# Optimization experiments

Measured on AMD Instinct MI355X. Metric: run time of the kernel, lower is better.

The kernel has to match this reference:

```python
import jax, jax.numpy as jnp
import numpy as np

N_NODES = 110
C = 4096  # in_channels = hidden = out_channels


def setup_inputs() -> dict:
    key = jax.random.key(0)
    ks = jax.random.split(key, 8)
    x = jax.random.normal(ks[0], (N_NODES, C), dtype=jnp.float32)
    adj = jax.random.randint(ks[1], (N_NODES, N_NODES), 0, 2, dtype=jnp.int32)
    # torch.nn.Linear weights stored [out_features, in_features]
    W2 = jax.random.normal(ks[2], (C, C), dtype=jnp.float32) / np.sqrt(C)
    b2 = jax.random.normal(ks[3], (C,), dtype=jnp.float32) * 0.01
    W1 = jax.random.normal(ks[4], (2 * C, C), dtype=jnp.float32) / np.sqrt(2 * C)
    b1 = jax.random.normal(ks[5], (C,), dtype=jnp.float32) * 0.01
    Wl = jax.random.normal(ks[6], (N_NODES, N_NODES), dtype=jnp.float32) / np.sqrt(N_NODES)
    bl = jax.random.normal(ks[7], (N_NODES,), dtype=jnp.float32) * 0.01
    # note: W1 is stored [in=2C, out=C]; W2 [in=C, out=C]; Wl [in=110, out=110]
    return {"x": x, "adj": adj, "W2": W2, "b2": b2, "W1": W1, "b1": b1, "Wl": Wl, "bl": bl}


def reference(x, adj, W2, b2, W1, b1, Wl, bl):
    # FeatGraphConv: h = lin2(x)
    h = x @ W2 + b2  # [N, C]
    # edge_index.nonzero(): adjacency -> edge list (i=src, j=dst); mean-aggregate
    # h[src] at dst. Dense equivalent: column-normalized mask matmul.
    mask = (adj != 0).astype(x.dtype)  # [N, N]
    deg = mask.sum(axis=0)  # in-degree of each target node j
    aggr = (mask.T @ h) / jnp.maximum(deg, 1.0)[:, None]  # [N, C]; 0 for isolated nodes (PyG mean)
    # update: lin1(cat(h, aggr)) then relu (in RegGNN.forward)
    out = jax.nn.relu(jnp.concatenate([h, aggr], axis=1) @ W1 + b1)  # [N, C]
    # x.t(); lin(110,110); x.t()
    out = (out.T @ Wl.T + bl).T  # [N, C]
    return out
```

## Files before the change

### kernel.cpp

```cpp
#include <hip/hip_runtime.h>
#include <hip/hip_fp16.h>

#define C 4096
#define NN 110
#define MPAD 112
#define NMT 7
#define KBS (NMT * 512)

typedef _Float16 f16x8 __attribute__((ext_vector_type(8)));
typedef float fx4 __attribute__((ext_vector_type(4)));
typedef unsigned long long ull;


__global__ __launch_bounds__(256)
void prep1_kernel(const float* __restrict__ x, _Float16* __restrict__ A1t) {
    int u = blockIdx.x * 256 + threadIdx.x;
    int kb  = u / 448;
    int rem = u - kb * 448;
    int mt  = rem >> 6;
    int L   = rem & 63;
    int n   = mt * 16 + (L & 15);
    int c   = kb * 32 + (L >> 4) * 8;
    f16x8 hv;
    if (n < NN) {
        float4 v0 = *(const float4*)(x + (size_t)n * C + c);
        float4 v1 = *(const float4*)(x + (size_t)n * C + c + 4);
        hv[0]=(_Float16)v0.x; hv[1]=(_Float16)v0.y; hv[2]=(_Float16)v0.z; hv[3]=(_Float16)v0.w;
        hv[4]=(_Float16)v1.x; hv[5]=(_Float16)v1.y; hv[6]=(_Float16)v1.z; hv[7]=(_Float16)v1.w;
    } else {
        for (int e = 0; e < 8; ++e) hv[e] = (_Float16)0.f;
    }
    *(f16x8*)(A1t + (size_t)u * 8) = hv;
}

__global__ __launch_bounds__(128)
void maskprep_kernel(const int* __restrict__ adj, ull* __restrict__ mlo,
                     ull* __restrict__ mhi, float* __restrict__ degs) {
    int j = threadIdx.x;
    if (j < NN) {
        ull lo = 0, hi = 0; int dg = 0;
        for (int i = 0; i < 64; ++i) {
            int m = (adj[i * NN + j] != 0);
            lo |= ((ull)m) << i; dg += m;
        }
        for (int i = 64; i < NN; ++i) {
            int m = (adj[i * NN + j] != 0);
            hi |= ((ull)m) << (i - 64); dg += m;
        }
        mlo[j] = lo; mhi[j] = hi;
        degs[j] = (float)(dg > 0 ? dg : 1);
    }
}

#define PIPE_BARRIER()                                                \
    do {                                                              \
        asm volatile("s_waitcnt lgkmcnt(0)" ::: "memory");            \
        __builtin_amdgcn_s_barrier();                                 \
        __builtin_amdgcn_sched_barrier(0);                            \
    } while (0)

template<int NITER>
__global__ __launch_bounds__(256, 3)
void mm_kernel(const _Float16* __restrict__ A, const float* __restrict__ B,
               float* __restrict__ Cacc) {
    __shared__ __align__(16) _Float16 As[2][2 * KBS];
    __shared__ __align__(16) _Float16 Bs[2][64 * 64];

    const int t   = threadIdx.x;
    const int j0  = blockIdx.x * 64;
    const int kb0 = blockIdx.y * (NITER * 2);
    const int w   = t >> 6;
    const int L   = t & 63;
    const int l15 = L & 15;
    const int q   = L >> 4;
    const int sc2 = (t & 31) * 2;
    const int kgr = (t >> 5) & 7;

    fx4 acc[7];
#pragma unroll
    for (int mt = 0; mt < 7; ++mt) acc[mt] = (fx4){0.f, 0.f, 0.f, 0.f};

    const float*    Bp  = B + (size_t)blockIdx.y * (NITER * 64) * C + j0 + sc2;
    const _Float16* ApC = A + (size_t)kb0 * KBS;
    const _Float16* BsR = &Bs[0][0] + (w * 16 + l15) * 64;
    const _Float16* AsR = &As[0][0];

    f16x8  av[4];
    float2 bva[8], bvb[8];

#define LOADA(ch)                                                              \
    { _Pragma("unroll")                                                        \
      for (int i = 0; i < 4; ++i)                                              \
          if (i < 3 || t < 128)                                                \
              av[i] = *(const f16x8*)(ApC + (size_t)(ch) * (2 * KBS)           \
                                      + (t + i * 256) * 8); }

#define COMMITA(buf)                                                           \
    { _Pragma("unroll")                                                        \
      for (int i = 0; i < 4; ++i)                                              \
          if (i < 3 || t < 128)                                                \
              *(f16x8*)(&As[buf][0] + (t + i * 256) * 8) = av[i]; }

#define LOADB(dst, ch)                                                         \
    { _Pragma("unroll")                                                        \
      for (int p = 0; p < 8; ++p)                                              \
          dst[p] = *(const float2*)(Bp + (size_t)((ch) * 64 + kgr * 8 + p) * C); }

#define COMMITB(src, buf)                                                      \
    { f16x8 h0, h1;                                                            \
      _Pragma("unroll")                                                        \
      for (int e = 0; e < 8; ++e) { h0[e] = (_Float16)src[e].x;                \
                                    h1[e] = (_Float16)src[e].y; }              \
      *(f16x8*)(&Bs[buf][0] + sc2 * 64 + ((kgr ^ (sc2 & 7)) << 3)) = h0;       \
      *(f16x8*)(&Bs[buf][0] + (sc2 + 1) * 64 + ((kgr ^ ((sc2 + 1) & 7)) << 3)) = h1; }

    LOADA(0);
    LOADB(bva, 0);
    COMMITA(0);
    COMMITB(bva, 0);
    LOADB(bva, 1);
    PIPE_BARRIER();

#pragma unroll
    for (int it = 0; it < NITER; ++it) {
        if (it + 1 < NITER) LOADA(it + 1);
        __builtin_amdgcn_sched_barrier(0);
        if (it + 2 < NITER) {
            if (it & 1) { LOADB(bva, it + 2); } else { LOADB(bvb, it + 2); }
        }
        __builtin_amdgcn_sched_barrier(0);
#pragma unroll
        for (int s = 0; s < 2; ++s) {
            f16x8 bf = *(const f16x8*)(BsR + (it & 1) * 4096
                            + ((((s << 2) + q) ^ (l15 & 7)) << 3));
#pragma unroll
            for (int mt = 0; mt < 7; ++mt) {
                f16x8 afrag = *(const f16x8*)(AsR + (it & 1) * (2 * KBS)
                                  + (s * 7 + mt) * 512 + L * 8);
                acc[mt] = __builtin_amdgcn_mfma_f32_16x16x32_f16(
                    afrag, bf, acc[mt], 0, 0, 0);
            }
        }
        if (it + 1 < NITER) {
            COMMITA((it + 1) & 1);
            if (it & 1) { COMMITB(bvb, (it + 1) & 1); }
            else        { COMMITB(bva, (it + 1) & 1); }
            PIPE_BARRIER();
        }
    }

    const int col = j0 + w * 16 + l15;
#pragma unroll
    for (int mt = 0; mt < 7; ++mt)
#pragma unroll
        for (int r = 0; r < 4; ++r) {
            int row = mt * 16 + q * 4 + r;
            if (row < NN)
                atomicAdd(&Cacc[(size_t)row * C + col], acc[mt][r]);
        }
#undef LOADA
#undef COMMITA
#undef LOADB
#undef COMMITB
}

__device__ __forceinline__ size_t fragidx(int n, int c) {
    return (size_t)(c >> 5) * KBS + (n >> 4) * 512
         + (((c >> 3) & 3) * 16 + (n & 15)) * 8 + (c & 7);
}

__global__ __launch_bounds__(256)
void agg_kernel(const float* __restrict__ h_raw, const ull* __restrict__ gmlo,
                const ull* __restrict__ gmhi, const float* __restrict__ gdegs,
                const float* __restrict__ b2, _Float16* __restrict__ A3t) {
    __shared__ float hb[NN * 16];
    const int t  = threadIdx.x;
    const int c0 = blockIdx.x * 16;

    for (int idx = t; idx < NN * 8; idx += 256) {
        int n = idx >> 3, cp = (idx & 7) << 1;
        float2 v = *(const float2*)(h_raw + (size_t)n * C + c0 + cp);
        float v0 = v.x + b2[c0 + cp];
        float v1 = v.y + b2[c0 + cp + 1];
        hb[n * 16 + cp]     = v0;
        hb[n * 16 + cp + 1] = v1;
        union { _Float16 h[2]; unsigned u; } pk;
        pk.h[0] = (_Float16)v0;
        pk.h[1] = (_Float16)v1;
        *(unsigned*)(A3t + fragidx(n, c0 + cp)) = pk.u;
    }
    if (t < 32) {
        int n  = 110 + ((t >> 3) & 1);
        int hs = t >> 4;
        int cp = (t & 7) << 1;
        *(unsigned*)(A3t + fragidx(n, hs * C + c0 + cp)) = 0u;
    }
    __syncthreads();
    for (int idx = t; idx < NN * 8; idx += 256) {
        int j = idx >> 3, cp = (idx & 7) << 1;
        ull lo = gmlo[j], hi = gmhi[j];
        float dg = gdegs[j];
        float a0 = 0.f, a1 = 0.f;
        for (int i = 0; i < 64; ++i)
            if ((lo >> i) & 1) { a0 += hb[i * 16 + cp]; a1 += hb[i * 16 + cp + 1]; }
        for (int i = 64; i < NN; ++i)
            if ((hi >> (i - 64)) & 1) { a0 += hb[i * 16 + cp]; a1 += hb[i * 16 + cp + 1]; }
        union { _Float16 h[2]; unsigned u; } pk;
        pk.h[0] = (_Float16)(a0 / dg);
        pk.h[1] = (_Float16)(a1 / dg);
        *(unsigned*)(A3t + fragidx(j, C + c0 + cp)) = pk.u;
    }
}

__global__ __launch_bounds__(256)
void fin_kernel(const float* __restrict__ z_raw, const float* __restrict__ b1,
                const float* __restrict__ Wl, const float* __restrict__ bl,
                float* __restrict__ out) {
    __shared__ float zs[NN * 64];
    const int t  = threadIdx.x;
    const int c0 = blockIdx.x * 64;
    const int c  = t & 63;

    for (int idx = t; idx < NN * 64; idx += 256) {
        int k = idx >> 6, cc = idx & 63;
        float v = z_raw[(size_t)k * C + c0 + cc] + b1[c0 + cc];
        zs[idx] = fmaxf(v, 0.f);
    }
    __syncthreads();
    for (int jj = 0; jj < 7; ++jj) {
        int j = blockIdx.y * 28 + jj * 4 + (t >> 6);
        if (j < NN) {
            float a = bl[j];
#pragma unroll 2
            for (int k = 0; k < NN; ++k)
                a += Wl[j * NN + k] * zs[k * 64 + c];
            out[(size_t)j * C + c0 + c] = a;
        }
    }
}

extern "C" void kernel_launch(void* const* d_in, const int* in_sizes, int n_in,
                              void* d_out, int out_size, void* d_ws, size_t ws_size,
                              hipStream_t stream) {
    const float* x   = (const float*)d_in[0];
    const int*   adj = (const int*)d_in[1];
    const float* W2  = (const float*)d_in[2];
    const float* b2  = (const float*)d_in[3];
    const float* W1  = (const float*)d_in[4];
    const float* b1  = (const float*)d_in[5];
    const float* Wl  = (const float*)d_in[6];
    const float* bl  = (const float*)d_in[7];
    float* out = (float*)d_out;

    char* ws = (char*)d_ws;
    float*    h_raw = (float*)(ws);
    float*    z_raw = (float*)(ws + 1802240);
    _Float16* A1t   = (_Float16*)(ws + 3604480);
    _Float16* A3t   = (_Float16*)(ws + 4521984);
    ull*      mlo   = (ull*)(ws + 6356992);
    ull*      mhi   = (ull*)(ws + 6357872);
    float*    degs  = (float*)(ws + 6358752);

    hipMemsetAsync(d_ws, 0, 3604480, stream);
    prep1_kernel<<<224, 256, 0, stream>>>(x, A1t);
    maskprep_kernel<<<1, 128, 0, stream>>>(adj, mlo, mhi, degs);
    mm_kernel<4><<<dim3(64, 16), 256, 0, stream>>>(A1t, W2, h_raw);
    agg_kernel<<<C / 16, 256, 0, stream>>>(h_raw, mlo, mhi, degs, b2, A3t);
    mm_kernel<8><<<dim3(64, 16), 256, 0, stream>>>(A3t, W1, z_raw);
    fin_kernel<<<dim3(C / 64, 4), 256, 0, stream>>>(z_raw, b1, Wl, bl, out);
}
```

Baseline: 355.5 us.

## Replace atomic split-K accumulation with per-slice partial buffers and reduction

The GEMM kernels now write split-K partial results into separate per-slice buffers with plain stores instead of atomicAdd into a zeroed accumulator. The split-K factor drops from 16 to 8, so each block does twice the K iterations. The partials are summed in the aggregation kernel for the first GEMM and in a new reduction kernel for the second. This removes the memset and the atomic contention, but adds an extra kernel launch, more partial-buffer traffic, and halves the grid size (512 blocks), which may leave the device underoccupied.

```diff
diff --git a/kernel.cpp b/kernel.cpp
--- a/kernel.cpp
+++ b/kernel.cpp
@@ -6,6 +6,7 @@
 #define MPAD 112
 #define NMT 7
 #define KBS (NMT * 512)
+#define NSLICE 8
 
 typedef _Float16 f16x8 __attribute__((ext_vector_type(8)));
 typedef float fx4 __attribute__((ext_vector_type(4)));
@@ -62,13 +63,12 @@
 template<int NITER>
 __global__ __launch_bounds__(256, 3)
 void mm_kernel(const _Float16* __restrict__ A, const float* __restrict__ B,
-               float* __restrict__ Cacc) {
+               float* __restrict__ Cpart) {
     __shared__ __align__(16) _Float16 As[2][2 * KBS];
     __shared__ __align__(16) _Float16 Bs[2][64 * 64];
 
     const int t   = threadIdx.x;
     const int j0  = blockIdx.x * 64;
-    const int kb0 = blockIdx.y * (NITER * 2);
     const int w   = t >> 6;
     const int L   = t & 63;
     const int l15 = L & 15;
@@ -81,7 +81,7 @@
     for (int mt = 0; mt < 7; ++mt) acc[mt] = (fx4){0.f, 0.f, 0.f, 0.f};
 
     const float*    Bp  = B + (size_t)blockIdx.y * (NITER * 64) * C + j0 + sc2;
-    const _Float16* ApC = A + (size_t)kb0 * KBS;
+    const _Float16* ApC = A + (size_t)blockIdx.y * (NITER * 2) * KBS;
     const _Float16* BsR = &Bs[0][0] + (w * 16 + l15) * 64;
     const _Float16* AsR = &As[0][0];
 
@@ -149,14 +149,14 @@
         }
     }
 
-    const int col = j0 + w * 16 + l15;
+    float* Cp = Cpart + (size_t)blockIdx.y * (NN * C) + j0 + w * 16 + l15;
 #pragma unroll
     for (int mt = 0; mt < 7; ++mt)
 #pragma unroll
         for (int r = 0; r < 4; ++r) {
             int row = mt * 16 + q * 4 + r;
             if (row < NN)
-                atomicAdd(&Cacc[(size_t)row * C + col], acc[mt][r]);
+                Cp[(size_t)row * C] = acc[mt][r];
         }
 #undef LOADA
 #undef COMMITA
@@ -170,7 +170,7 @@
 }
 
 __global__ __launch_bounds__(256)
-void agg_kernel(const float* __restrict__ h_raw, const ull* __restrict__ gmlo,
+void agg_kernel(const float* __restrict__ hpart, const ull* __restrict__ gmlo,
                 const ull* __restrict__ gmhi, const float* __restrict__ gdegs,
                 const float* __restrict__ b2, _Float16* __restrict__ A3t) {
     __shared__ float hb[NN * 16];
@@ -179,9 +179,13 @@
 
     for (int idx = t; idx < NN * 8; idx += 256) {
         int n = idx >> 3, cp = (idx & 7) << 1;
-        float2 v = *(const float2*)(h_raw + (size_t)n * C + c0 + cp);
-        float v0 = v.x + b2[c0 + cp];
-        float v1 = v.y + b2[c0 + cp + 1];
+        float v0 = b2[c0 + cp], v1 = b2[c0 + cp + 1];
+#pragma unroll
+        for (int p = 0; p < NSLICE; ++p) {
+            float2 v = *(const float2*)(hpart + (size_t)p * (NN * C)
+                                        + (size_t)n * C + c0 + cp);
+            v0 += v.x; v1 += v.y;
+        }
         hb[n * 16 + cp]     = v0;
         hb[n * 16 + cp + 1] = v1;
         union { _Float16 h[2]; unsigned u; } pk;
@@ -213,6 +217,20 @@
 }
 
 __global__ __launch_bounds__(256)
+void zred_kernel(const float* __restrict__ zpart, float* __restrict__ z_raw) {
+    int idx = blockIdx.x * 256 + threadIdx.x;
+    if (idx < NN * (C / 4)) {
+        fx4 s = (fx4){0.f, 0.f, 0.f, 0.f};
+#pragma unroll
+        for (int p = 0; p < NSLICE; ++p) {
+            fx4 v = *(const fx4*)(zpart + (size_t)p * (NN * C) + (size_t)idx * 4);
+            s.x += v.x; s.y += v.y; s.z += v.z; s.w += v.w;
+        }
+        *(fx4*)(z_raw + (size_t)idx * 4) = s;
+    }
+}
+
+__global__ __launch_bounds__(256)
 void fin_kernel(const float* __restrict__ z_raw, const float* __restrict__ b1,
                 const float* __restrict__ Wl, const float* __restrict__ bl,
                 float* __restrict__ out) {
@@ -253,19 +271,20 @@
     float* out = (float*)d_out;
 
     char* ws = (char*)d_ws;
-    float*    h_raw = (float*)(ws);
-    float*    z_raw = (float*)(ws + 1802240);
-    _Float16* A1t   = (_Float16*)(ws + 3604480);
-    _Float16* A3t   = (_Float16*)(ws + 4521984);
-    ull*      mlo   = (ull*)(ws + 6356992);
-    ull*      mhi   = (ull*)(ws + 6357872);
-    float*    degs  = (float*)(ws + 6358752);
-
-    hipMemsetAsync(d_ws, 0, 3604480, stream);
+    float*    hpart = (float*)(ws);
+    float*    zpart = (float*)(ws + 14417920);
+    float*    z_raw = (float*)(ws + 28835840);
+    _Float16* A1t   = (_Float16*)(ws + 30638080);
+    _Float16* A3t   = (_Float16*)(ws + 31555584);
+    ull*      mlo   = (ull*)(ws + 33390592);
+    ull*      mhi   = (ull*)(ws + 33391472);
+    float*    degs  = (float*)(ws + 33392352);
+
     prep1_kernel<<<224, 256, 0, stream>>>(x, A1t);
     maskprep_kernel<<<1, 128, 0, stream>>>(adj, mlo, mhi, degs);
-    mm_kernel<4><<<dim3(64, 16), 256, 0, stream>>>(A1t, W2, h_raw);
-    agg_kernel<<<C / 16, 256, 0, stream>>>(h_raw, mlo, mhi, degs, b2, A3t);
-    mm_kernel<8><<<dim3(64, 16), 256, 0, stream>>>(A3t, W1, z_raw);
+    mm_kernel<8><<<dim3(64, NSLICE), 256, 0, stream>>>(A1t, W2, hpart);
+    agg_kernel<<<C / 16, 256, 0, stream>>>(hpart, mlo, mhi, degs, b2, A3t);
+    mm_kernel<16><<<dim3(64, NSLICE), 256, 0, stream>>>(A3t, W1, zpart);
+    zred_kernel<<<440, 256, 0, stream>>>(zpart, z_raw);
     fin_kernel<<<dim3(C / 64, 4), 256, 0, stream>>>(z_raw, b1, Wl, bl, out);
 }
```

Measured after the change: 352.1 us. Within noise of the previous version (-1.0%).

## Retile GEMM to 256-wide N tiles with register-resident A fragments

Applied to the files above, without the earlier changes.

The mm_kernel is restructured so that each block covers 256 output columns instead of 64, with a K chunk of 32 per iteration. A fragments are loaded straight from global memory into registers rather than staged through LDS, and B is staged as float4 reads converted to fp16 into a swizzled LDS tile. Each wave keeps a 7x4 grid of MFMA accumulators, so each B fragment read from LDS is reused across 7 M-tiles and each A fragment across 4 N-tiles. The mask-prep kernel is folded into an extra block of prep1 to save one launch. The cost is higher register pressure, so occupancy is lowered to 2 blocks per CU, and A is now read redundantly from global memory by every block.

```diff
diff --git a/kernel.cpp b/kernel.cpp
--- a/kernel.cpp
+++ b/kernel.cpp
@@ -3,7 +3,6 @@
 
 #define C 4096
 #define NN 110
-#define MPAD 112
 #define NMT 7
 #define KBS (NMT * 512)
 
@@ -11,9 +10,39 @@
 typedef float fx4 __attribute__((ext_vector_type(4)));
 typedef unsigned long long ull;
 
+__device__ __forceinline__ size_t fragidx(int n, int c) {
+    return (size_t)(c >> 5) * KBS + (n >> 4) * 512
+         + (((c >> 3) & 3) * 16 + (n & 15)) * 8 + (c & 7);
+}
+
+#define PIPE_BARRIER()                                                \
+    do {                                                              \
+        asm volatile("s_waitcnt lgkmcnt(0)" ::: "memory");            \
+        __builtin_amdgcn_s_barrier();                                 \
+        __builtin_amdgcn_sched_barrier(0);                            \
+    } while (0)
 
 __global__ __launch_bounds__(256)
-void prep1_kernel(const float* __restrict__ x, _Float16* __restrict__ A1t) {
+void prep1_kernel(const float* __restrict__ x, _Float16* __restrict__ A1t,
+                  const int* __restrict__ adj, ull* __restrict__ mlo,
+                  ull* __restrict__ mhi, float* __restrict__ degs) {
+    if (blockIdx.x == 224) {
+        int j = threadIdx.x;
+        if (j < NN) {
+            ull lo = 0, hi = 0; int dg = 0;
+            for (int i = 0; i < 64; ++i) {
+                int m = (adj[i * NN + j] != 0);
+                lo |= ((ull)m) << i; dg += m;
+            }
+            for (int i = 64; i < NN; ++i) {
+                int m = (adj[i * NN + j] != 0);
+                hi |= ((ull)m) << (i - 64); dg += m;
+            }
+            mlo[j] = lo; mhi[j] = hi;
+            degs[j] = (float)(dg > 0 ? dg : 1);
+        }
+        return;
+    }
     int u = blockIdx.x * 256 + threadIdx.x;
     int kb  = u / 448;
     int rem = u - kb * 448;
@@ -33,140 +62,95 @@
     *(f16x8*)(A1t + (size_t)u * 8) = hv;
 }
 
-__global__ __launch_bounds__(128)
-void maskprep_kernel(const int* __restrict__ adj, ull* __restrict__ mlo,
-                     ull* __restrict__ mhi, float* __restrict__ degs) {
-    int j = threadIdx.x;
-    if (j < NN) {
-        ull lo = 0, hi = 0; int dg = 0;
-        for (int i = 0; i < 64; ++i) {
-            int m = (adj[i * NN + j] != 0);
-            lo |= ((ull)m) << i; dg += m;
-        }
-        for (int i = 64; i < NN; ++i) {
-            int m = (adj[i * NN + j] != 0);
-            hi |= ((ull)m) << (i - 64); dg += m;
-        }
-        mlo[j] = lo; mhi[j] = hi;
-        degs[j] = (float)(dg > 0 ? dg : 1);
-    }
-}
-
-#define PIPE_BARRIER()                                                \
-    do {                                                              \
-        asm volatile("s_waitcnt lgkmcnt(0)" ::: "memory");            \
-        __builtin_amdgcn_s_barrier();                                 \
-        __builtin_amdgcn_sched_barrier(0);                            \
-    } while (0)
-
-template<int NITER>
-__global__ __launch_bounds__(256, 3)
+template<int NC>
+__global__ __launch_bounds__(256, 2)
 void mm_kernel(const _Float16* __restrict__ A, const float* __restrict__ B,
                float* __restrict__ Cacc) {
-    __shared__ __align__(16) _Float16 As[2][2 * KBS];
-    __shared__ __align__(16) _Float16 Bs[2][64 * 64];
+    __shared__ __align__(16) _Float16 Bs[2][256 * 32];
 
     const int t   = threadIdx.x;
-    const int j0  = blockIdx.x * 64;
-    const int kb0 = blockIdx.y * (NITER * 2);
+    const int n0  = blockIdx.x * 256;
+    const int y   = blockIdx.y;
     const int w   = t >> 6;
     const int L   = t & 63;
     const int l15 = L & 15;
     const int q   = L >> 4;
-    const int sc2 = (t & 31) * 2;
-    const int kgr = (t >> 5) & 7;
-
-    fx4 acc[7];
-#pragma unroll
-    for (int mt = 0; mt < 7; ++mt) acc[mt] = (fx4){0.f, 0.f, 0.f, 0.f};
-
-    const float*    Bp  = B + (size_t)blockIdx.y * (NITER * 64) * C + j0 + sc2;
-    const _Float16* ApC = A + (size_t)kb0 * KBS;
-    const _Float16* BsR = &Bs[0][0] + (w * 16 + l15) * 64;
-    const _Float16* AsR = &As[0][0];
-
-    f16x8  av[4];
-    float2 bva[8], bvb[8];
-
-#define LOADA(ch)                                                              \
-    { _Pragma("unroll")                                                        \
-      for (int i = 0; i < 4; ++i)                                              \
-          if (i < 3 || t < 128)                                                \
-              av[i] = *(const f16x8*)(ApC + (size_t)(ch) * (2 * KBS)           \
-                                      + (t + i * 256) * 8); }
-
-#define COMMITA(buf)                                                           \
-    { _Pragma("unroll")                                                        \
-      for (int i = 0; i < 4; ++i)                                              \
-          if (i < 3 || t < 128)                                                \
-              *(f16x8*)(&As[buf][0] + (t + i * 256) * 8) = av[i]; }
-
-#define LOADB(dst, ch)                                                         \
+    const int m   = t & 63;
+
+    fx4 acc[7][4];
+#pragma unroll
+    for (int mt = 0; mt < 7; ++mt)
+#pragma unroll
+        for (int nt = 0; nt < 4; ++nt)
+            acc[mt][nt] = (fx4){0.f, 0.f, 0.f, 0.f};
+
+    const float*    Bp  = B + (size_t)(y * NC * 32) * C + n0 + m * 4;
+    const _Float16* ApL = A + (size_t)(y * NC) * KBS + L * 8;
+    const _Float16* BsR = &Bs[0][0] + (w * 64) * 32;
+
+    fx4   bva[8];
+    f16x8 af[7];
+
+#define LOADB(kc)                                                              \
     { _Pragma("unroll")                                                        \
       for (int p = 0; p < 8; ++p)                                              \
-          dst[p] = *(const float2*)(Bp + (size_t)((ch) * 64 + kgr * 8 + p) * C); }
-
-#define COMMITB(src, buf)                                                      \
-    { f16x8 h0, h1;                                                            \
-      _Pragma("unroll")                                                        \
-      for (int e = 0; e < 8; ++e) { h0[e] = (_Float16)src[e].x;                \
-                                    h1[e] = (_Float16)src[e].y; }              \
-      *(f16x8*)(&Bs[buf][0] + sc2 * 64 + ((kgr ^ (sc2 & 7)) << 3)) = h0;       \
-      *(f16x8*)(&Bs[buf][0] + (sc2 + 1) * 64 + ((kgr ^ ((sc2 + 1) & 7)) << 3)) = h1; }
-
-    LOADA(0);
-    LOADB(bva, 0);
-    COMMITA(0);
-    COMMITB(bva, 0);
-    LOADB(bva, 1);
+          bva[p] = *(const fx4*)(Bp + (size_t)((kc) * 32 + w * 8 + p) * C); }
+
+#define COMMITB(buf)                                                           \
+    { _Pragma("unroll")                                                        \
+      for (int cj = 0; cj < 4; ++cj) {                                         \
+          f16x8 hv;                                                            \
+          _Pragma("unroll")                                                    \
+          for (int e = 0; e < 8; ++e) hv[e] = (_Float16)bva[e][cj];            \
+          *(f16x8*)(&Bs[buf][0] + (m * 4 + cj) * 32                            \
+                    + ((w ^ (m & 3)) << 3)) = hv;                              \
+      } }
+
+#define LOADAF(kc)                                                             \
+    { _Pragma("unroll")                                                        \
+      for (int mt = 0; mt < 7; ++mt)                                           \
+          af[mt] = *(const f16x8*)(ApL + (size_t)(kc) * KBS + mt * 512); }
+
+    LOADB(0);
+    COMMITB(0);
+    LOADAF(0);
     PIPE_BARRIER();
 
 #pragma unroll
-    for (int it = 0; it < NITER; ++it) {
-        if (it + 1 < NITER) LOADA(it + 1);
+    for (int it = 0; it < NC; ++it) {
+        if (it + 1 < NC) LOADB(it + 1);
         __builtin_amdgcn_sched_barrier(0);
-        if (it + 2 < NITER) {
-            if (it & 1) { LOADB(bva, it + 2); } else { LOADB(bvb, it + 2); }
-        }
-        __builtin_amdgcn_sched_barrier(0);
-#pragma unroll
-        for (int s = 0; s < 2; ++s) {
-            f16x8 bf = *(const f16x8*)(BsR + (it & 1) * 4096
-                            + ((((s << 2) + q) ^ (l15 & 7)) << 3));
-#pragma unroll
-            for (int mt = 0; mt < 7; ++mt) {
-                f16x8 afrag = *(const f16x8*)(AsR + (it & 1) * (2 * KBS)
-                                  + (s * 7 + mt) * 512 + L * 8);
-                acc[mt] = __builtin_amdgcn_mfma_f32_16x16x32_f16(
-                    afrag, bf, acc[mt], 0, 0, 0);
+#pragma unroll
+        for (int nt = 0; nt < 4; ++nt) {
+            f16x8 bf = *(const f16x8*)(BsR + (it & 1) * 8192 + (nt * 16 + l15) * 32
+                            + ((q ^ ((l15 >> 2) & 3)) << 3));
+#pragma unroll
+            for (int mt = 0; mt < 7; ++mt)
+                acc[mt][nt] = __builtin_amdgcn_mfma_f32_16x16x32_f16(
+                    af[mt], bf, acc[mt][nt], 0, 0, 0);
+        }
+        if (it + 1 < NC) {
+            LOADAF(it + 1);
+            COMMITB((it + 1) & 1);
+            PIPE_BARRIER();
+        }
+    }
+
+#pragma unroll
+    for (int mt = 0; mt < 7; ++mt)
+#pragma unroll
+        for (int nt = 0; nt < 4; ++nt) {
+            const int col = n0 + w * 64 + nt * 16 + l15;
+#pragma unroll
+            for (int r = 0; r < 4; ++r) {
+                int row = mt * 16 + q * 4 + r;
+                if (row < NN)
+                    atomicAdd(&Cacc[(size_t)row * C + col], acc[mt][nt][r]);
             }
         }
-        if (it + 1 < NITER) {
-            COMMITA((it + 1) & 1);
-            if (it & 1) { COMMITB(bvb, (it + 1) & 1); }
-            else        { COMMITB(bva, (it + 1) & 1); }
-            PIPE_BARRIER();
-        }
-    }
-
-    const int col = j0 + w * 16 + l15;
-#pragma unroll
-    for (int mt = 0; mt < 7; ++mt)
-#pragma unroll
-        for (int r = 0; r < 4; ++r) {
-            int row = mt * 16 + q * 4 + r;
-            if (row < NN)
-                atomicAdd(&Cacc[(size_t)row * C + col], acc[mt][r]);
-        }
-#undef LOADA
-#undef COMMITA
 #undef LOADB
 #undef COMMITB
-}
-
-__device__ __forceinline__ size_t fragidx(int n, int c) {
-    return (size_t)(c >> 5) * KBS + (n >> 4) * 512
-         + (((c >> 3) & 3) * 16 + (n & 15)) * 8 + (c & 7);
+#undef LOADAF
 }
 
 __global__ __launch_bounds__(256)
@@ -262,10 +246,9 @@
     float*    degs  = (float*)(ws + 6358752);
 
     hipMemsetAsync(d_ws, 0, 3604480, stream);
-    prep1_kernel<<<224, 256, 0, stream>>>(x, A1t);
-    maskprep_kernel<<<1, 128, 0, stream>>>(adj, mlo, mhi, degs);
-    mm_kernel<4><<<dim3(64, 16), 256, 0, stream>>>(A1t, W2, h_raw);
+    prep1_kernel<<<225, 256, 0, stream>>>(x, A1t, adj, mlo, mhi, degs);
+    mm_kernel<4><<<dim3(16, 32), 256, 0, stream>>>(A1t, W2, h_raw);
     agg_kernel<<<C / 16, 256, 0, stream>>>(h_raw, mlo, mhi, degs, b2, A3t);
-    mm_kernel<8><<<dim3(64, 16), 256, 0, stream>>>(A3t, W1, z_raw);
+    mm_kernel<8><<<dim3(16, 32), 256, 0, stream>>>(A3t, W1, z_raw);
     fin_kernel<<<dim3(C / 64, 4), 256, 0, stream>>>(z_raw, b1, Wl, bl, out);
 }
```

New measurement: 420.9 us. 1.18x slower.
